# Performance work log

Measured on AMD Instinct MI355X. Metric: run time of the kernel, lower is better.

## Reference

```python
import jax, jax.numpy as jnp
import numpy as np

ALPHA = 0.2  # LeakyReLU negative slope
NEG_INF = -9e15


def setup_inputs() -> dict:
    key = jax.random.key(0)
    k1, k2, k3, k4 = jax.random.split(key, 4)
    N, Fin, Fout = 8192, 256, 64
    h = jax.random.normal(k1, (N, Fin), dtype=jnp.float32)
    adj = jax.random.randint(k2, (N, N), 0, 2, dtype=jnp.int32)
    # xavier_uniform with gain=1.414
    def xavier(k, shape, gain=1.414):
        fan_in, fan_out = shape[0], shape[1]
        bound = gain * np.sqrt(6.0 / (fan_in + fan_out))
        return jax.random.uniform(k, shape, jnp.float32, -bound, bound)
    W = xavier(k3, (Fin, Fout))
    a = xavier(k4, (2 * Fout, 1))
    return {"h": h, "adj": adj, "W": W, "a": a}


def reference(h, adj, W, a):
    Fout = W.shape[1]
    Wh = h @ W                                  # [N, Fout]
    Wh1 = Wh @ a[:Fout, :]                      # [N, 1]
    Wh2 = Wh @ a[Fout:, :]                      # [N, 1]
    e = jax.nn.leaky_relu(Wh1 + Wh2.T, negative_slope=ALPHA)  # [N, N]
    attention = jnp.where(adj > 0, e, NEG_INF)
    attention = jax.nn.softmax(attention, axis=1)
    h_prime = attention @ Wh                    # [N, Fout]
    return jax.nn.elu(h_prime)
```

## Files before the change

### kernel.cpp

```cpp
#include <hip/hip_runtime.h>
#include <hip/hip_bf16.h>
#include <math.h>

#define NN 8192
#define FIN 256
#define FOUT 64
#define LRELU_ALPHA 0.2f
#define TI 16
#define TJ 256
#define JS 4
#define JCHUNK (NN / JS)

typedef __attribute__((ext_vector_type(8))) short short8v;
typedef __attribute__((ext_vector_type(4))) float f32x4;

static __device__ inline unsigned short f2bf(float f) {
  __hip_bfloat16 b = __float2bfloat16(f);
  return *reinterpret_cast<unsigned short*>(&b);
}


__global__ __launch_bounds__(256) void gat_prep(
    const float* __restrict__ W, const float* __restrict__ a,
    unsigned short* __restrict__ WF, float* __restrict__ wa1,
    float* __restrict__ wa2) {
  const int t = threadIdx.x;
  if (blockIdx.x < 8) {
    const int wid = blockIdx.x * 4 + (t >> 6);
    const int ks = wid >> 2, nt = wid & 3;
    const int l = t & 63;
    const int kg = l >> 4, nn = l & 15;
    unsigned short frag[8];
#pragma unroll
    for (int e = 0; e < 8; ++e) {
      frag[e] = f2bf(W[(ks * 32 + kg * 8 + e) * FOUT + nt * 16 + nn]);
    }
    *(short8v*)&WF[wid * 512 + l * 8] = *(short8v*)frag;
  } else {
    float s1 = 0.f, s2 = 0.f;
#pragma unroll 4
    for (int c = 0; c < FOUT; c += 4) {
      const float4 wv = *(const float4*)&W[t * FOUT + c];
      const float4 a1 = *(const float4*)&a[c];
      const float4 a2 = *(const float4*)&a[FOUT + c];
      s1 += wv.x * a1.x + wv.y * a1.y + wv.z * a1.z + wv.w * a1.w;
      s2 += wv.x * a2.x + wv.y * a2.y + wv.z * a2.z + wv.w * a2.w;
    }
    wa1[t] = s1;
    wa2[t] = s2;
  }
}

__global__ __launch_bounds__(256) void gat_wh5(
    const float* __restrict__ h, const unsigned short* __restrict__ WF,
    const float* __restrict__ wa1, const float* __restrict__ wa2,
    unsigned short* __restrict__ WhF, float* __restrict__ Wh1,
    float* __restrict__ Wh2) {
  __shared__ __align__(16) float hs[TI][260];

  const int t = threadIdx.x;
  const int i0 = blockIdx.x * TI;

#pragma unroll
  for (int q = 0; q < 4; ++q) {
    const int idx = q * 256 + t;
    const float4 v = *(const float4*)&h[(size_t)i0 * FIN + (size_t)idx * 4];
    const int row = idx >> 6, col = (idx & 63) * 4;
    *(float4*)&hs[row][col] = v;
  }
  __syncthreads();

  {
    const int row = t >> 4, s = t & 15;
    float p1 = 0.f, p2 = 0.f;
#pragma unroll
    for (int q = 0; q < 16; ++q) {
      const int k = s + q * 16;
      const float hv = hs[row][k];
      p1 = fmaf(hv, wa1[k], p1);
      p2 = fmaf(hv, wa2[k], p2);
    }
#pragma unroll
    for (int off = 8; off; off >>= 1) {
      p1 += __shfl_xor(p1, off);
      p2 += __shfl_xor(p2, off);
    }
    if (s == 0) {
      Wh1[i0 + row] = p1;
      Wh2[i0 + row] = p2;
    }
  }

  const int w = t >> 6, l = t & 63;
  const int kg = l >> 4, m = l & 15;
  f32x4 acc = {0.f, 0.f, 0.f, 0.f};
#pragma unroll
  for (int ks = 0; ks < 8; ++ks) {
    const float4 fa = *(const float4*)&hs[m][ks * 32 + kg * 8];
    const float4 fb = *(const float4*)&hs[m][ks * 32 + kg * 8 + 4];
    unsigned short af[8];
    af[0] = f2bf(fa.x); af[1] = f2bf(fa.y);
    af[2] = f2bf(fa.z); af[3] = f2bf(fa.w);
    af[4] = f2bf(fb.x); af[5] = f2bf(fb.y);
    af[6] = f2bf(fb.z); af[7] = f2bf(fb.w);
    const short8v bf = *(const short8v*)&WF[(ks * 4 + w) * 512 + l * 8];
    acc =
        __builtin_amdgcn_mfma_f32_16x16x32_bf16(*(short8v*)af, bf, acc, 0, 0, 0);
  }

  const int k0 = i0 + kg * 4;
  const int col = w * 16 + m;
  const int basef = ((k0 >> 5) * 4 + (col >> 4)) * 512 +
                    (((k0 >> 3) & 3) * 16 + (col & 15)) * 8 + (k0 & 7);
  ushort4 st;
  st.x = f2bf(acc[0]);
  st.y = f2bf(acc[1]);
  st.z = f2bf(acc[2]);
  st.w = f2bf(acc[3]);
  *(ushort4*)&WhF[basef] = st;
}

__global__ __launch_bounds__(256) void gat_attn4(
    const int* __restrict__ adj, const unsigned short* __restrict__ WhF,
    const float* __restrict__ Wh1, const float* __restrict__ Wh2,
    float* __restrict__ num, float* __restrict__ den) {
  __shared__ __align__(16) unsigned short p_lds[2][TI * TJ];
  __shared__ float den_lds[TI];

  const int t = threadIdx.x;
  const int jsplit = blockIdx.x & (JS - 1);
  const int i0 = (blockIdx.x >> 2) * TI;
  const int j0 = jsplit * JCHUNK;

  const int r0 = t >> 5;
  const int col8 = (t & 31) * 8;
  const float w1_0 = Wh1[i0 + r0];
  const float w1_1 = Wh1[i0 + r0 + 8];

  const int w = t >> 6;
  const int l = t & 63;
  const int arow = l & 15;
  const int kg = l >> 4;
  const int colw = w * 16 + arow;

  float ds0 = 0.f, ds1 = 0.f;
  f32x4 acc = {0.f, 0.f, 0.f, 0.f};

  const int wr0 = ((r0 * TJ + col8) * 2) ^ ((r0 & 7) << 4);
  const int wr1 = (((r0 + 8) * TJ + col8) * 2) ^ ((r0 & 7) << 4);
  const int rdb = (arow * TJ * 2) ^ ((arow & 7) << 4);

  int4 a00, a01, a10, a11;
  float4 w2a, w2b;
  {
    const int4* ap0 = (const int4*)&adj[(size_t)(i0 + r0) * NN + j0 + col8];
    const int4* ap1 = (const int4*)&adj[(size_t)(i0 + r0 + 8) * NN + j0 + col8];
    a00 = ap0[0]; a01 = ap0[1];
    a10 = ap1[0]; a11 = ap1[1];
    w2a = *(const float4*)&Wh2[j0 + col8];
    w2b = *(const float4*)&Wh2[j0 + col8 + 4];
  }

  for (int jb = j0, it = 0; jb < j0 + JCHUNK; jb += TJ, ++it) {
    unsigned short* pl = &p_lds[it & 1][0];

    const float w2v[8] = {w2a.x, w2a.y, w2a.z, w2a.w,
                          w2b.x, w2b.y, w2b.z, w2b.w};
    const int am0[8] = {a00.x, a00.y, a00.z, a00.w, a01.x, a01.y, a01.z, a01.w};
    const int am1[8] = {a10.x, a10.y, a10.z, a10.w, a11.x, a11.y, a11.z, a11.w};

    short8v pv0, pv1;
#pragma unroll
    for (int e = 0; e < 8; ++e) {
      float v0 = w1_0 + w2v[e];
      v0 = v0 > 0.f ? v0 : LRELU_ALPHA * v0;
      float p0 = (am0[e] > 0) ? __expf(v0) : 0.f;
      ds0 += p0;
      pv0[e] = (short)f2bf(p0);
      float v1 = w1_1 + w2v[e];
      v1 = v1 > 0.f ? v1 : LRELU_ALPHA * v1;
      float p1 = (am1[e] > 0) ? __expf(v1) : 0.f;
      ds1 += p1;
      pv1[e] = (short)f2bf(p1);
    }
    *(short8v*)((char*)pl + wr0) = pv0;
    *(short8v*)((char*)pl + wr1) = pv1;

    if (jb + TJ < j0 + JCHUNK) {
      const int jn = jb + TJ;
      const int4* ap0 = (const int4*)&adj[(size_t)(i0 + r0) * NN + jn + col8];
      const int4* ap1 =
          (const int4*)&adj[(size_t)(i0 + r0 + 8) * NN + jn + col8];
      a00 = ap0[0]; a01 = ap0[1];
      a10 = ap1[0]; a11 = ap1[1];
      w2a = *(const float4*)&Wh2[jn + col8];
      w2b = *(const float4*)&Wh2[jn + col8 + 4];
    }

    asm volatile("s_waitcnt lgkmcnt(0)" ::: "memory");
    __builtin_amdgcn_sched_barrier(0);
    __builtin_amdgcn_s_barrier();

    const int kblk0 = jb >> 5;
#pragma unroll
    for (int kt = 0; kt < 8; ++kt) {
      short8v af = *(const short8v*)((const char*)pl +
                                     (rdb ^ ((kt * 32 + kg * 8) * 2)));
      short8v bf = *(const short8v*)&WhF[((kblk0 + kt) * 4 + w) * 512 + l * 8];
      acc = __builtin_amdgcn_mfma_f32_16x16x32_bf16(af, bf, acc, 0, 0, 0);
    }
  }

#pragma unroll
  for (int off = 16; off; off >>= 1) {
    ds0 += __shfl_xor(ds0, off);
    ds1 += __shfl_xor(ds1, off);
  }
  if ((t & 31) == 0) {
    const int rr = t >> 5;
    den_lds[rr] = ds0;
    den_lds[rr + 8] = ds1;
  }
  __syncthreads();
  if (t < TI) den[jsplit * NN + i0 + t] = den_lds[t];

#pragma unroll
  for (int r = 0; r < 4; ++r) {
    num[(size_t)(jsplit * NN + i0 + kg * 4 + r) * FOUT + colw] = acc[r];
  }
}

__global__ __launch_bounds__(256) void gat_comb(
    const float* __restrict__ num, const float* __restrict__ den,
    float* __restrict__ out) {
  const int idx = blockIdx.x * 256 + threadIdx.x;
  const int row = idx >> 6;
  float n = 0.f, d = 0.f;
#pragma unroll
  for (int s = 0; s < JS; ++s) {
    n += num[(size_t)s * NN * FOUT + idx];
    d += den[s * NN + row];
  }
  float v = n / d;
  out[idx] = v > 0.f ? v : expm1f(v);
}

extern "C" void kernel_launch(void* const* d_in, const int* in_sizes, int n_in,
                              void* d_out, int out_size, void* d_ws,
                              size_t ws_size, hipStream_t stream) {
  const float* h = (const float*)d_in[0];
  const int* adj = (const int*)d_in[1];
  const float* W = (const float*)d_in[2];
  const float* a = (const float*)d_in[3];
  float* out = (float*)d_out;

  unsigned short* WhF = (unsigned short*)d_ws;
  float* Wh1 = (float*)((char*)d_ws + (1 << 20));
  float* Wh2 = Wh1 + NN;
  float* num = Wh2 + NN;
  float* den = num + (size_t)JS * NN * FOUT;
  unsigned short* WF = (unsigned short*)((char*)d_ws + (16u << 20));
  float* wa1 = (float*)((char*)d_ws + (16u << 20) + (64u << 10));
  float* wa2 = wa1 + FIN;

  gat_prep<<<9, 256, 0, stream>>>(W, a, WF, wa1, wa2);
  gat_wh5<<<NN / TI, 256, 0, stream>>>(h, WF, wa1, wa2, WhF, Wh1, Wh2);
  gat_attn4<<<(NN / TI) * JS, 256, 0, stream>>>(adj, WhF, Wh1, Wh2, num, den);
  gat_comb<<<NN * FOUT / 256, 256, 0, stream>>>(num, den, out);
}
```

Measured before the change: 87.76 us.

## Restructure attention kernel to 32x32 MFMA with per-wave register P tiles

The attention kernel now uses 32-row tiles and 32x32x16 bf16 MFMAs. Each wave builds its probability fragment directly in registers from its own adjacency loads, so the LDS P tile and the per-tile barrier are gone. Each of the four waves covers a different j sub-range, and the partial accumulators are reduced through LDS at the end. Adjacency loads are double-buffered in registers, and the Wh projection is stored in a new fragment layout to match. This removes LDS round-trips and syncs in the main loop, at the cost of more registers and an extra cross-wave reduction.

```diff
diff --git a/kernel.cpp b/kernel.cpp
--- a/kernel.cpp
+++ b/kernel.cpp
@@ -7,12 +7,14 @@
 #define FOUT 64
 #define LRELU_ALPHA 0.2f
 #define TI 16
+#define TIB 32
 #define TJ 256
 #define JS 4
 #define JCHUNK (NN / JS)
 
 typedef __attribute__((ext_vector_type(8))) short short8v;
 typedef __attribute__((ext_vector_type(4))) float f32x4;
+typedef __attribute__((ext_vector_type(16))) float f32x16;
 
 static __device__ inline unsigned short f2bf(float f) {
   __hip_bfloat16 b = __float2bfloat16(f);
@@ -51,10 +53,10 @@
   }
 }
 
-__global__ __launch_bounds__(256) void gat_wh5(
+__global__ __launch_bounds__(256) void gat_wh6(
     const float* __restrict__ h, const unsigned short* __restrict__ WF,
     const float* __restrict__ wa1, const float* __restrict__ wa2,
-    unsigned short* __restrict__ WhF, float* __restrict__ Wh1,
+    unsigned short* __restrict__ WhB, float* __restrict__ Wh1,
     float* __restrict__ Wh2) {
   __shared__ __align__(16) float hs[TI][260];
 
@@ -108,125 +110,112 @@
         __builtin_amdgcn_mfma_f32_16x16x32_bf16(*(short8v*)af, bf, acc, 0, 0, 0);
   }
 
-  const int k0 = i0 + kg * 4;
-  const int col = w * 16 + m;
-  const int basef = ((k0 >> 5) * 4 + (col >> 4)) * 512 +
-                    (((k0 >> 3) & 3) * 16 + (col & 15)) * 8 + (k0 & 7);
-  ushort4 st;
-  st.x = f2bf(acc[0]);
-  st.y = f2bf(acc[1]);
-  st.z = f2bf(acc[2]);
-  st.w = f2bf(acc[3]);
-  *(ushort4*)&WhF[basef] = st;
-}
-
-__global__ __launch_bounds__(256) void gat_attn4(
-    const int* __restrict__ adj, const unsigned short* __restrict__ WhF,
+  {
+    const int jk = i0 >> 4;
+    const int lam = (kg >> 1) * 32 + (w & 1) * 16 + m;
+    const int off = (jk * 2 + (w >> 1)) * 512 + lam * 8 + (kg & 1) * 4;
+    ushort4 st;
+    st.x = f2bf(acc[0]);
+    st.y = f2bf(acc[1]);
+    st.z = f2bf(acc[2]);
+    st.w = f2bf(acc[3]);
+    *(ushort4*)&WhB[off] = st;
+  }
+}
+
+__global__ __launch_bounds__(256) void gat_attn5(
+    const int* __restrict__ adj, const unsigned short* __restrict__ WhB,
     const float* __restrict__ Wh1, const float* __restrict__ Wh2,
     float* __restrict__ num, float* __restrict__ den) {
-  __shared__ __align__(16) unsigned short p_lds[2][TI * TJ];
-  __shared__ float den_lds[TI];
+  __shared__ float red[4][TIB][FOUT];
+  __shared__ float dred[4][TIB];
 
   const int t = threadIdx.x;
+  const int w = t >> 6, l = t & 63;
+  const int row = l & 31, hi = l >> 5;
   const int jsplit = blockIdx.x & (JS - 1);
-  const int i0 = (blockIdx.x >> 2) * TI;
+  const int i0 = (blockIdx.x >> 2) * TIB;
   const int j0 = jsplit * JCHUNK;
-
-  const int r0 = t >> 5;
-  const int col8 = (t & 31) * 8;
-  const float w1_0 = Wh1[i0 + r0];
-  const float w1_1 = Wh1[i0 + r0 + 8];
-
-  const int w = t >> 6;
-  const int l = t & 63;
-  const int arow = l & 15;
-  const int kg = l >> 4;
-  const int colw = w * 16 + arow;
-
-  float ds0 = 0.f, ds1 = 0.f;
-  f32x4 acc = {0.f, 0.f, 0.f, 0.f};
-
-  const int wr0 = ((r0 * TJ + col8) * 2) ^ ((r0 & 7) << 4);
-  const int wr1 = (((r0 + 8) * TJ + col8) * 2) ^ ((r0 & 7) << 4);
-  const int rdb = (arow * TJ * 2) ^ ((arow & 7) << 4);
-
-  int4 a00, a01, a10, a11;
-  float4 w2a, w2b;
-  {
-    const int4* ap0 = (const int4*)&adj[(size_t)(i0 + r0) * NN + j0 + col8];
-    const int4* ap1 = (const int4*)&adj[(size_t)(i0 + r0 + 8) * NN + j0 + col8];
-    a00 = ap0[0]; a01 = ap0[1];
-    a10 = ap1[0]; a11 = ap1[1];
-    w2a = *(const float4*)&Wh2[j0 + col8];
-    w2b = *(const float4*)&Wh2[j0 + col8 + 4];
-  }
-
-  for (int jb = j0, it = 0; jb < j0 + JCHUNK; jb += TJ, ++it) {
-    unsigned short* pl = &p_lds[it & 1][0];
-
-    const float w2v[8] = {w2a.x, w2a.y, w2a.z, w2a.w,
-                          w2b.x, w2b.y, w2b.z, w2b.w};
-    const int am0[8] = {a00.x, a00.y, a00.z, a00.w, a01.x, a01.y, a01.z, a01.w};
-    const int am1[8] = {a10.x, a10.y, a10.z, a10.w, a11.x, a11.y, a11.z, a11.w};
-
-    short8v pv0, pv1;
-#pragma unroll
-    for (int e = 0; e < 8; ++e) {
-      float v0 = w1_0 + w2v[e];
-      v0 = v0 > 0.f ? v0 : LRELU_ALPHA * v0;
-      float p0 = (am0[e] > 0) ? __expf(v0) : 0.f;
-      ds0 += p0;
-      pv0[e] = (short)f2bf(p0);
-      float v1 = w1_1 + w2v[e];
-      v1 = v1 > 0.f ? v1 : LRELU_ALPHA * v1;
-      float p1 = (am1[e] > 0) ? __expf(v1) : 0.f;
-      ds1 += p1;
-      pv1[e] = (short)f2bf(p1);
-    }
-    *(short8v*)((char*)pl + wr0) = pv0;
-    *(short8v*)((char*)pl + wr1) = pv1;
-
-    if (jb + TJ < j0 + JCHUNK) {
-      const int jn = jb + TJ;
-      const int4* ap0 = (const int4*)&adj[(size_t)(i0 + r0) * NN + jn + col8];
-      const int4* ap1 =
-          (const int4*)&adj[(size_t)(i0 + r0 + 8) * NN + jn + col8];
-      a00 = ap0[0]; a01 = ap0[1];
-      a10 = ap1[0]; a11 = ap1[1];
-      w2a = *(const float4*)&Wh2[jn + col8];
-      w2b = *(const float4*)&Wh2[jn + col8 + 4];
-    }
-
-    asm volatile("s_waitcnt lgkmcnt(0)" ::: "memory");
-    __builtin_amdgcn_sched_barrier(0);
-    __builtin_amdgcn_s_barrier();
-
-    const int kblk0 = jb >> 5;
-#pragma unroll
-    for (int kt = 0; kt < 8; ++kt) {
-      short8v af = *(const short8v*)((const char*)pl +
-                                     (rdb ^ ((kt * 32 + kg * 8) * 2)));
-      short8v bf = *(const short8v*)&WhF[((kblk0 + kt) * 4 + w) * 512 + l * 8];
-      acc = __builtin_amdgcn_mfma_f32_16x16x32_bf16(af, bf, acc, 0, 0, 0);
-    }
-  }
-
-#pragma unroll
-  for (int off = 16; off; off >>= 1) {
-    ds0 += __shfl_xor(ds0, off);
-    ds1 += __shfl_xor(ds1, off);
-  }
-  if ((t & 31) == 0) {
-    const int rr = t >> 5;
-    den_lds[rr] = ds0;
-    den_lds[rr + 8] = ds1;
+  const int row_g = i0 + row;
+  const int* __restrict__ arow = adj + (size_t)row_g * NN;
+  const float w1 = Wh1[row_g];
+  const int jwb = 64 * w + hi * 8;
+
+  f32x16 acc0 = {0.f, 0.f, 0.f, 0.f, 0.f, 0.f, 0.f, 0.f,
+                 0.f, 0.f, 0.f, 0.f, 0.f, 0.f, 0.f, 0.f};
+  f32x16 acc1 = acc0;
+  float dsum = 0.f;
+
+  int4 ajA[8], ajB[8];
+
+#define LOADT(DST, JB)                                              \
+  {                                                                 \
+    _Pragma("unroll") for (int s = 0; s < 4; ++s) {                 \
+      const int4* _p = (const int4*)&arow[(JB) + jwb + s * 16];     \
+      DST[2 * s] = _p[0];                                           \
+      DST[2 * s + 1] = _p[1];                                       \
+    }                                                               \
+  }
+
+#define TILE(AJ, JB)                                                          \
+  {                                                                           \
+    _Pragma("unroll") for (int s = 0; s < 4; ++s) {                           \
+      const int jj = (JB) + jwb + s * 16;                                     \
+      const float4 w2a = *(const float4*)&Wh2[jj];                            \
+      const float4 w2b = *(const float4*)&Wh2[jj + 4];                        \
+      const float w2v[8] = {w2a.x, w2a.y, w2a.z, w2a.w,                       \
+                            w2b.x, w2b.y, w2b.z, w2b.w};                      \
+      const int am[8] = {AJ[2 * s].x,     AJ[2 * s].y,     AJ[2 * s].z,       \
+                         AJ[2 * s].w,     AJ[2 * s + 1].x, AJ[2 * s + 1].y,   \
+                         AJ[2 * s + 1].z, AJ[2 * s + 1].w};                   \
+      short8v af;                                                             \
+      _Pragma("unroll") for (int e = 0; e < 8; ++e) {                         \
+        float v = w1 + w2v[e];                                                \
+        v = v > 0.f ? v : LRELU_ALPHA * v;                                    \
+        float p = (am[e] > 0) ? __expf(v) : 0.f;                              \
+        dsum += p;                                                            \
+        af[e] = (short)f2bf(p);                                               \
+      }                                                                       \
+      const int jk2 = (((JB) + 64 * w + s * 16) >> 4) * 2;                    \
+      const short8v b0 = *(const short8v*)&WhB[(size_t)(jk2 + 0) * 512 + l * 8]; \
+      const short8v b1 = *(const short8v*)&WhB[(size_t)(jk2 + 1) * 512 + l * 8]; \
+      acc0 = __builtin_amdgcn_mfma_f32_32x32x16_bf16(af, b0, acc0, 0, 0, 0);  \
+      acc1 = __builtin_amdgcn_mfma_f32_32x32x16_bf16(af, b1, acc1, 0, 0, 0);  \
+    }                                                                         \
+  }
+
+  LOADT(ajA, j0);
+#pragma unroll 1
+  for (int it = 0; it < 8; it += 2) {
+    const int jb0 = j0 + it * TJ;
+    LOADT(ajB, jb0 + TJ);
+    TILE(ajA, jb0);
+    if (it + 2 < 8) LOADT(ajA, jb0 + 2 * TJ);
+    TILE(ajB, jb0 + TJ);
+  }
+#undef LOADT
+#undef TILE
+
+  dsum += __shfl_xor(dsum, 32);
+  if (hi == 0) dred[w][row] = dsum;
+
+#pragma unroll
+  for (int r = 0; r < 16; ++r) {
+    const int orow = (r & 3) + 8 * (r >> 2) + 4 * hi;
+    red[w][orow][row] = acc0[r];
+    red[w][orow][32 + row] = acc1[r];
   }
   __syncthreads();
-  if (t < TI) den[jsplit * NN + i0 + t] = den_lds[t];
-
-#pragma unroll
-  for (int r = 0; r < 4; ++r) {
-    num[(size_t)(jsplit * NN + i0 + kg * 4 + r) * FOUT + colw] = acc[r];
+
+  for (int idx = t; idx < TIB * FOUT; idx += 256) {
+    const int orow = idx >> 6, oc = idx & 63;
+    const float s =
+        red[0][orow][oc] + red[1][orow][oc] + red[2][orow][oc] + red[3][orow][oc];
+    num[(size_t)(jsplit * NN + i0 + orow) * FOUT + oc] = s;
+  }
+  if (t < TIB) {
+    den[jsplit * NN + i0 + t] =
+        dred[0][t] + dred[1][t] + dred[2][t] + dred[3][t];
   }
 }
 
@@ -254,7 +243,7 @@
   const float* a = (const float*)d_in[3];
   float* out = (float*)d_out;
 
-  unsigned short* WhF = (unsigned short*)d_ws;
+  unsigned short* WhB = (unsigned short*)d_ws;
   float* Wh1 = (float*)((char*)d_ws + (1 << 20));
   float* Wh2 = Wh1 + NN;
   float* num = Wh2 + NN;
@@ -264,7 +253,7 @@
   float* wa2 = wa1 + FIN;
 
   gat_prep<<<9, 256, 0, stream>>>(W, a, WF, wa1, wa2);
-  gat_wh5<<<NN / TI, 256, 0, stream>>>(h, WF, wa1, wa2, WhF, Wh1, Wh2);
-  gat_attn4<<<(NN / TI) * JS, 256, 0, stream>>>(adj, WhF, Wh1, Wh2, num, den);
+  gat_wh6<<<NN / TI, 256, 0, stream>>>(h, WF, wa1, wa2, WhB, Wh1, Wh2);
+  gat_attn5<<<(NN / TIB) * JS, 256, 0, stream>>>(adj, WhB, Wh1, Wh2, num, den);
   gat_comb<<<NN * FOUT / 256, 256, 0, stream>>>(num, den, out);
 }
```

New measurement: 113.5 us. +29.3%, slower.
